# Performance work log

Measured on AMD Instinct MI355X. Metric: run time of the kernel, lower is better.

Reference implementation:

```python
import jax, jax.numpy as jnp
import numpy as np

N_USERS = 100000
N_ITEMS = 50000
N_ENTITIES = 180000
N_USER_NODES = 150000  # n_users + n_attributes
N_REL = 32
D = 64


def scatter_mean(src, index, num_segments):
    # torch_scatter scatter_mean: sum / count.clamp(min=1)
    s = jax.ops.segment_sum(src, index, num_segments=num_segments)
    cnt = jax.ops.segment_sum(jnp.ones((src.shape[0],), src.dtype), index, num_segments=num_segments)
    return s / jnp.clip(cnt, 1.0)[:, None]


def setup_inputs() -> dict:
    key = jax.random.key(0)
    ks = jax.random.split(key, 12)
    return {
        "entity_emb": jax.random.normal(ks[0], (N_ENTITIES, D), jnp.float32),
        "user_emb": jax.random.normal(ks[1], (N_USER_NODES, D), jnp.float32),
        "weight": jax.random.normal(ks[2], (N_REL, D), jnp.float32) * 0.1,
        "gate1_w": jax.random.normal(ks[3], (D, D), jnp.float32) * 0.1,
        "gate2_w": jax.random.normal(ks[4], (D, D), jnp.float32) * 0.1,
        "gate3_w": jax.random.normal(ks[5], (D, D), jnp.float32) * 0.1,
        "edge_index": jax.random.randint(ks[6], (2, 1500000), 0, N_ENTITIES, jnp.int32),
        "edge_type": jax.random.randint(ks[7], (1500000,), 0, N_REL, jnp.int32),
        "user_edge_index": jax.random.randint(ks[8], (2, 1000000), 0, N_USER_NODES, jnp.int32),
        "user_edge_type": jax.random.randint(ks[9], (1000000,), 0, N_REL, jnp.int32),
        "mat_row": jax.random.randint(ks[10], (1500000,), 0, N_USERS, jnp.int32),
        "mat_col": jax.random.randint(ks[11], (1500000,), 0, N_ITEMS, jnp.int32),
    }


def reference(entity_emb, user_emb, weight, gate1_w, gate2_w, gate3_w,
              edge_index, edge_type, user_edge_index, user_edge_type,
              mat_row, mat_col):
    # KG aggregate: gather tail + relation, multiply, scatter-mean to head
    head, tail = edge_index[0], edge_index[1]
    entity_agg = scatter_mean(entity_emb[tail] * weight[edge_type], head, N_ENTITIES)

    # UKG aggregate over the user+attribute graph
    uhead, utail = user_edge_index[0], user_edge_index[1]
    attribute_agg = scatter_mean(user_emb[utail] * weight[user_edge_type], uhead, N_USER_NODES)

    # user_gate: fuse KG item aggregation with user->item interaction aggregation
    item_kg_agg = entity_agg[:N_ITEMS]
    i_u_agg = scatter_mean(user_emb[mat_row] * weight[0], mat_col, N_ITEMS)
    gi = jax.nn.sigmoid(item_kg_agg @ gate1_w.T + i_u_agg @ gate2_w.T)
    item_emb_fusion = gi * item_kg_agg + (1.0 - gi) * i_u_agg

    # item_gate: fuse UKG user aggregation with item->user interaction aggregation
    user_ukg_agg = attribute_agg[:N_USERS]
    u_i_agg = scatter_mean(entity_emb[mat_col] * weight[0], mat_row, N_USERS)
    hi = jax.nn.sigmoid(u_i_agg @ gate2_w.T + user_ukg_agg @ gate3_w.T)
    user_emb_fusion = hi * user_ukg_agg + (1.0 - hi) * u_i_agg

    # forward output: fused item/user blocks concatenated with untouched tails
    entity_out = jnp.concatenate([item_emb_fusion, entity_agg[N_ITEMS:]], axis=0)
    user_out = jnp.concatenate([user_emb_fusion, attribute_agg[N_USERS:]], axis=0)
    return entity_out, user_out
```

## Files before the change

kernel.cpp:

```cpp
#include <hip/hip_runtime.h>

#define DD 64
#define NBKT 1024
#define CHUNK 8192
#define CAP_B 6656

struct SegCfg {
    int qbase[4];
    int rpb[4];
    float inv[4];
    int soff[4];
    int rows[4];
};

__global__ void __launch_bounds__(512, 2)
split_kernel(const int* __restrict__ dA, const int* __restrict__ sA, const int* __restrict__ tA,
             const int* __restrict__ dB, const int* __restrict__ sB, const int* __restrict__ tB,
             const int* __restrict__ dC, const int* __restrict__ sC,
             const int* __restrict__ dD, const int* __restrict__ sD,
             int nA, int nB, int nC, int nD,
             SegCfg cfg, int* __restrict__ gcur, unsigned long long* __restrict__ bkt) {
    __shared__ unsigned long long ord[CHUNK];
    __shared__ int cnt[NBKT];
    __shared__ int sc[NBKT];
    __shared__ int gb[NBKT];
    int t = threadIdx.x;
    int Etot = nA + nB + nC + nD;
    int base = blockIdx.x * CHUNK;
    if (base >= Etot) return;

    cnt[t] = 0; cnt[t + 512] = 0;
    __syncthreads();

    unsigned long long val[16];
    int qv[16], rv[16];
#pragma unroll
    for (int k = 0; k < 16; ++k) {
        int i = base + k * 512 + t;
        qv[k] = -1;
        if (i < Etot) {
            int j = i, d, seg, pv;
            if (j < nA)              { seg = 0; d = dA[j]; pv = sA[j] | (tA[j] << 20); }
            else if ((j -= nA) < nB) { seg = 1; d = dB[j]; pv = sB[j] | (tB[j] << 20); }
            else if ((j -= nB) < nC) { seg = 2; d = dC[j]; pv = sC[j]; }
            else { j -= nC;            seg = 3; d = dD[j]; pv = sD[j]; }
            int rpb = cfg.rpb[seg];
            int q = (int)((float)d * cfg.inv[seg]);
            if (d >= (q + 1) * rpb) ++q;
            else if (d < q * rpb) --q;
            int g = d + cfg.soff[seg];
            q += cfg.qbase[seg];
            val[k] = ((unsigned long long)q << 44) | ((unsigned long long)g << 25) | (unsigned)pv;
            qv[k] = q;
            rv[k] = atomicAdd(&cnt[q], 1);
        }
    }
    __syncthreads();

    int c0 = cnt[2 * t], c1 = cnt[2 * t + 1];
    {
        int s2 = c0 + c1;
        gb[t] = s2;
        __syncthreads();
        for (int off = 1; off < 512; off <<= 1) {
            int x = (t >= off) ? gb[t - off] : 0;
            __syncthreads();
            gb[t] += x;
            __syncthreads();
        }
        int run = gb[t] - s2;
        sc[2 * t] = run;
        sc[2 * t + 1] = run + c0;
    }
    __syncthreads();
    gb[2 * t]     = c0 ? atomicAdd(&gcur[2 * t], c0) : 0;
    gb[2 * t + 1] = c1 ? atomicAdd(&gcur[2 * t + 1], c1) : 0;
    __syncthreads();

#pragma unroll
    for (int k = 0; k < 16; ++k)
        if (qv[k] >= 0) ord[sc[qv[k]] + rv[k]] = val[k];
    __syncthreads();

    int tot = sc[NBKT - 1] + cnt[NBKT - 1];
    for (int i = t; i < tot; i += 512) {
        unsigned long long v = ord[i];
        int q = (int)(v >> 44);
        int idx = gb[q] + (i - sc[q]);
        if (idx < CAP_B)
            bkt[(size_t)q * CAP_B + idx] = v & 0xFFFFFFFFFFFULL;
    }
}

__global__ void __launch_bounds__(512, 2)
sort_gather(const unsigned long long* __restrict__ bkt, const int* __restrict__ gcur,
            SegCfg cfg,
            const float* __restrict__ entity_emb, const float* __restrict__ user_emb,
            const float* __restrict__ weight,
            float* __restrict__ out, float* __restrict__ usr_out,
            float* __restrict__ iu, float* __restrict__ ui) {
    __shared__ int cnt[1024];
    __shared__ int part[512];
    __shared__ int stage[CAP_B];
    int b = blockIdx.x, t = threadIdx.x;

    int seg = 0;
    if (b >= cfg.qbase[3]) seg = 3;
    else if (b >= cfg.qbase[2]) seg = 2;
    else if (b >= cfg.qbase[1]) seg = 1;
    int lb = b - cfg.qbase[seg];
    int row0 = cfg.soff[seg] + lb * cfg.rpb[seg];
    int nr = cfg.rows[seg] - lb * cfg.rpb[seg];
    if (nr > cfg.rpb[seg]) nr = cfg.rpb[seg];
    int n = gcur[b];
    if (n > CAP_B) n = CAP_B;
    const unsigned long long* src = bkt + (size_t)b * CAP_B;

    const float* emb = (seg == 0 || seg == 3) ? entity_emb : user_emb;
    float* dbase;
    if (seg == 0)      dbase = out     + (size_t)row0 * DD;
    else if (seg == 1) dbase = usr_out + (size_t)(row0 - cfg.soff[1]) * DD;
    else if (seg == 2) dbase = iu      + (size_t)(row0 - cfg.soff[2]) * DD;
    else               dbase = ui      + (size_t)(row0 - cfg.soff[3]) * DD;

    cnt[t] = 0; cnt[t + 512] = 0;
    __syncthreads();
    for (int i = t; i < n; i += 512) {
        int g = (int)(src[i] >> 25);
        atomicAdd(&cnt[g - row0], 1);
    }
    __syncthreads();

    {
        int c0 = cnt[2 * t], c1 = cnt[2 * t + 1];
        int s2 = c0 + c1;
        part[t] = s2;
        __syncthreads();
        for (int off = 1; off < 512; off <<= 1) {
            int y = (t >= off) ? part[t - off] : 0;
            __syncthreads();
            part[t] += y;
            __syncthreads();
        }
        int run = part[t] - s2;
        cnt[2 * t] = run;
        cnt[2 * t + 1] = run + c0;
    }
    __syncthreads();

    for (int i = t; i < n; i += 512) {
        unsigned long long v = src[i];
        int lr = (int)(v >> 25) - row0;
        int pos = atomicAdd(&cnt[lr], 1);
        stage[pos] = (int)(v & 0x1FFFFFF);
    }
    __syncthreads();

    int wv = t >> 6, lane = t & 63;
    for (int r = wv; r < nr; r += 8) {
        int start = (r == 0) ? 0 : cnt[r - 1];
        int end = cnt[r];
        float acc = 0.f;
        for (int base = start; base < end; base += 64) {
            int m = end - base; if (m > 64) m = 64;
            int pv = (lane < m) ? stage[base + lane] : 0;
            int j = 0;
            for (; j + 4 <= m; j += 4) {
                int p0 = __builtin_amdgcn_readlane(pv, j);
                int p1 = __builtin_amdgcn_readlane(pv, j + 1);
                int p2 = __builtin_amdgcn_readlane(pv, j + 2);
                int p3 = __builtin_amdgcn_readlane(pv, j + 3);
                const float* r0 = emb + (((unsigned)p0 & 0xFFFFFu) << 6);
                const float* r1 = emb + (((unsigned)p1 & 0xFFFFFu) << 6);
                const float* r2 = emb + (((unsigned)p2 & 0xFFFFFu) << 6);
                const float* r3 = emb + (((unsigned)p3 & 0xFFFFFu) << 6);
                float e0 = r0[lane], w0 = weight[(((unsigned)p0 >> 20) << 6) + lane];
                float e1 = r1[lane], w1 = weight[(((unsigned)p1 >> 20) << 6) + lane];
                float e2 = r2[lane], w2 = weight[(((unsigned)p2 >> 20) << 6) + lane];
                float e3 = r3[lane], w3 = weight[(((unsigned)p3 >> 20) << 6) + lane];
                acc += e0 * w0; acc += e1 * w1; acc += e2 * w2; acc += e3 * w3;
            }
            for (; j < m; ++j) {
                int pj = __builtin_amdgcn_readlane(pv, j);
                const float* rj = emb + (((unsigned)pj & 0xFFFFFu) << 6);
                acc += rj[lane] * weight[(((unsigned)pj >> 20) << 6) + lane];
            }
        }
        int deg = end - start;
        dbase[(size_t)r * DD + lane] = acc / (float)(deg > 0 ? deg : 1);
    }
}

__global__ void __launch_bounds__(256)
gate_fuse_kernel(const float* __restrict__ a_, const float* __restrict__ b_,
                 const float* __restrict__ gA, const float* __restrict__ gB,
                 float* __restrict__ out, int n_rows) {
    int lane = threadIdx.x & 63;
    float wa[DD], wb[DD];
    {
        const float4* ga4 = (const float4*)(gA + (lane << 6));
        const float4* gb4 = (const float4*)(gB + (lane << 6));
#pragma unroll
        for (int k4 = 0; k4 < 16; ++k4) {
            float4 va = ga4[k4];
            float4 vb = gb4[k4];
            wa[4 * k4 + 0] = va.x; wa[4 * k4 + 1] = va.y;
            wa[4 * k4 + 2] = va.z; wa[4 * k4 + 3] = va.w;
            wb[4 * k4 + 0] = vb.x; wb[4 * k4 + 1] = vb.y;
            wb[4 * k4 + 2] = vb.z; wb[4 * k4 + 3] = vb.w;
        }
    }
    int wid = blockIdx.x * (blockDim.x >> 6) + (threadIdx.x >> 6);
    int nw = gridDim.x * (blockDim.x >> 6);
    for (int row = wid; row < n_rows; row += nw) {
        int row_s = __builtin_amdgcn_readfirstlane(row);
        const float* ar = a_ + ((size_t)row_s << 6);
        const float* br = b_ + ((size_t)row_s << 6);
        float z = 0.f;
#pragma unroll
        for (int k = 0; k < DD; ++k) z = fmaf(ar[k], wa[k], z);
#pragma unroll
        for (int k = 0; k < DD; ++k) z = fmaf(br[k], wb[k], z);
        float g = 1.f / (1.f + expf(-z));
        float av = ar[lane], bv = br[lane];
        out[((size_t)row_s << 6) + lane] = g * av + (1.f - g) * bv;
    }
}

extern "C" void kernel_launch(void* const* d_in, const int* in_sizes, int n_in,
                              void* d_out, int out_size, void* d_ws, size_t ws_size,
                              hipStream_t stream) {
    const float* entity_emb = (const float*)d_in[0];
    const float* user_emb   = (const float*)d_in[1];
    const float* weight     = (const float*)d_in[2];
    const float* g1         = (const float*)d_in[3];
    const float* g2         = (const float*)d_in[4];
    const float* g3         = (const float*)d_in[5];
    const int* edge_index  = (const int*)d_in[6];
    const int* edge_type   = (const int*)d_in[7];
    const int* uedge_index = (const int*)d_in[8];
    const int* uedge_type  = (const int*)d_in[9];
    const int* mat_row     = (const int*)d_in[10];
    const int* mat_col     = (const int*)d_in[11];

    const int n_entities   = in_sizes[0] / DD;
    const int n_user_nodes = in_sizes[1] / DD;
    const int nA           = in_sizes[7];
    const int nB           = in_sizes[9];
    const int nM           = in_sizes[10];
    const int n_items      = 50000;
    const int n_users      = 100000;

    const int offB = n_entities;
    const int offC = offB + n_user_nodes;
    const int offD = offC + n_items;
    const int Etot = nA + nB + nM + nM;

    float* out      = (float*)d_out;
    float* user_out = out + (size_t)n_entities * DD;

    unsigned long long* bkt = (unsigned long long*)d_ws;
    int* gcur = (int*)(bkt + (size_t)NBKT * CAP_B);
    float* iu = (float*)(gcur + NBKT);
    float* ui = iu + (size_t)n_items * DD;

    SegCfg cfg;
    {
        int nb[4];
        nb[0] = (int)((long long)nA * NBKT / Etot);
        nb[1] = (int)((long long)nB * NBKT / Etot);
        nb[2] = (int)((long long)nM * NBKT / Etot);
        nb[3] = NBKT - nb[0] - nb[1] - nb[2];
        int rows[4] = {n_entities, n_user_nodes, n_items, n_users};
        int soff[4] = {0, offB, offC, offD};
        int qb = 0;
        for (int s = 0; s < 4; ++s) {
            cfg.qbase[s] = qb;
            cfg.rpb[s]   = (rows[s] + nb[s] - 1) / nb[s];
            cfg.inv[s]   = 1.0f / (float)cfg.rpb[s];
            cfg.soff[s]  = soff[s];
            cfg.rows[s]  = rows[s];
            qb += nb[s];
        }
    }

    hipMemsetAsync(gcur, 0, NBKT * sizeof(int), stream);

    int nchunk = (Etot + CHUNK - 1) / CHUNK;
    split_kernel<<<nchunk, 512, 0, stream>>>(edge_index, edge_index + nA, edge_type,
                                             uedge_index, uedge_index + nB, uedge_type,
                                             mat_col, mat_row,
                                             mat_row, mat_col,
                                             nA, nB, nM, nM, cfg, gcur, bkt);
    sort_gather<<<NBKT, 512, 0, stream>>>(bkt, gcur, cfg,
                                          entity_emb, user_emb, weight,
                                          out, user_out, iu, ui);

    gate_fuse_kernel<<<1024, 256, 0, stream>>>(out, iu, g1, g2, out, n_items);
    gate_fuse_kernel<<<1024, 256, 0, stream>>>(user_out, ui, g3, g2, user_out, n_users);
}
```

Measured before the change: 564.5 us.

## Two-pass bucket split without LDS staging to raise split_kernel occupancy

Rewrites split_kernel as two passes over the edge chunk. The first pass only counts entries per bucket, then the block reserves global ranges with atomics, and the second pass re-reads the inputs and writes each entry straight to its bucket slot using a shared per-bucket cursor. This removes the 64KB shared ordering buffer, the block-wide prefix scan and the per-thread register arrays, so the launch bound can go from 2 to 8 blocks per CU. The cost is reading the index arrays twice and losing the coalesced, bucket-ordered global writes.

```diff
diff --git a/kernel.cpp b/kernel.cpp
--- a/kernel.cpp
+++ b/kernel.cpp
@@ -13,16 +13,15 @@
     int rows[4];
 };
 
-__global__ void __launch_bounds__(512, 2)
+__global__ void __launch_bounds__(512, 8)
 split_kernel(const int* __restrict__ dA, const int* __restrict__ sA, const int* __restrict__ tA,
              const int* __restrict__ dB, const int* __restrict__ sB, const int* __restrict__ tB,
              const int* __restrict__ dC, const int* __restrict__ sC,
              const int* __restrict__ dD, const int* __restrict__ sD,
              int nA, int nB, int nC, int nD,
              SegCfg cfg, int* __restrict__ gcur, unsigned long long* __restrict__ bkt) {
-    __shared__ unsigned long long ord[CHUNK];
     __shared__ int cnt[NBKT];
-    __shared__ int sc[NBKT];
+    __shared__ int cur[NBKT];
     __shared__ int gb[NBKT];
     int t = threadIdx.x;
     int Etot = nA + nB + nC + nD;
@@ -30,65 +29,50 @@
     if (base >= Etot) return;
 
     cnt[t] = 0; cnt[t + 512] = 0;
-    __syncthreads();
-
-    unsigned long long val[16];
-    int qv[16], rv[16];
-#pragma unroll
+    cur[t] = 0; cur[t + 512] = 0;
+    __syncthreads();
+
     for (int k = 0; k < 16; ++k) {
         int i = base + k * 512 + t;
-        qv[k] = -1;
-        if (i < Etot) {
-            int j = i, d, seg, pv;
-            if (j < nA)              { seg = 0; d = dA[j]; pv = sA[j] | (tA[j] << 20); }
-            else if ((j -= nA) < nB) { seg = 1; d = dB[j]; pv = sB[j] | (tB[j] << 20); }
-            else if ((j -= nB) < nC) { seg = 2; d = dC[j]; pv = sC[j]; }
-            else { j -= nC;            seg = 3; d = dD[j]; pv = sD[j]; }
-            int rpb = cfg.rpb[seg];
-            int q = (int)((float)d * cfg.inv[seg]);
-            if (d >= (q + 1) * rpb) ++q;
-            else if (d < q * rpb) --q;
-            int g = d + cfg.soff[seg];
-            q += cfg.qbase[seg];
-            val[k] = ((unsigned long long)q << 44) | ((unsigned long long)g << 25) | (unsigned)pv;
-            qv[k] = q;
-            rv[k] = atomicAdd(&cnt[q], 1);
-        }
-    }
-    __syncthreads();
-
-    int c0 = cnt[2 * t], c1 = cnt[2 * t + 1];
-    {
-        int s2 = c0 + c1;
-        gb[t] = s2;
-        __syncthreads();
-        for (int off = 1; off < 512; off <<= 1) {
-            int x = (t >= off) ? gb[t - off] : 0;
-            __syncthreads();
-            gb[t] += x;
-            __syncthreads();
-        }
-        int run = gb[t] - s2;
-        sc[2 * t] = run;
-        sc[2 * t + 1] = run + c0;
-    }
-    __syncthreads();
-    gb[2 * t]     = c0 ? atomicAdd(&gcur[2 * t], c0) : 0;
-    gb[2 * t + 1] = c1 ? atomicAdd(&gcur[2 * t + 1], c1) : 0;
-    __syncthreads();
-
-#pragma unroll
-    for (int k = 0; k < 16; ++k)
-        if (qv[k] >= 0) ord[sc[qv[k]] + rv[k]] = val[k];
-    __syncthreads();
-
-    int tot = sc[NBKT - 1] + cnt[NBKT - 1];
-    for (int i = t; i < tot; i += 512) {
-        unsigned long long v = ord[i];
-        int q = (int)(v >> 44);
-        int idx = gb[q] + (i - sc[q]);
+        if (i >= Etot) break;
+        int j = i, d, seg;
+        if (j < nA)              { seg = 0; d = dA[j]; }
+        else if ((j -= nA) < nB) { seg = 1; d = dB[j]; }
+        else if ((j -= nB) < nC) { seg = 2; d = dC[j]; }
+        else { j -= nC;            seg = 3; d = dD[j]; }
+        int rpb = cfg.rpb[seg];
+        int q = (int)((float)d * cfg.inv[seg]);
+        if (d >= (q + 1) * rpb) ++q;
+        else if (d < q * rpb) --q;
+        atomicAdd(&cnt[q + cfg.qbase[seg]], 1);
+    }
+    __syncthreads();
+
+    {
+        int c0 = cnt[2 * t], c1 = cnt[2 * t + 1];
+        gb[2 * t]     = c0 ? atomicAdd(&gcur[2 * t], c0) : 0;
+        gb[2 * t + 1] = c1 ? atomicAdd(&gcur[2 * t + 1], c1) : 0;
+    }
+    __syncthreads();
+
+    for (int k = 0; k < 16; ++k) {
+        int i = base + k * 512 + t;
+        if (i >= Etot) break;
+        int j = i, d, seg, pv;
+        if (j < nA)              { seg = 0; d = dA[j]; pv = sA[j] | (tA[j] << 20); }
+        else if ((j -= nA) < nB) { seg = 1; d = dB[j]; pv = sB[j] | (tB[j] << 20); }
+        else if ((j -= nB) < nC) { seg = 2; d = dC[j]; pv = sC[j]; }
+        else { j -= nC;            seg = 3; d = dD[j]; pv = sD[j]; }
+        int rpb = cfg.rpb[seg];
+        int q = (int)((float)d * cfg.inv[seg]);
+        if (d >= (q + 1) * rpb) ++q;
+        else if (d < q * rpb) --q;
+        int g = d + cfg.soff[seg];
+        q += cfg.qbase[seg];
+        int pos = atomicAdd(&cur[q], 1);
+        int idx = gb[q] + pos;
         if (idx < CAP_B)
-            bkt[(size_t)q * CAP_B + idx] = v & 0xFFFFFFFFFFFULL;
+            bkt[(size_t)q * CAP_B + idx] = ((unsigned long long)g << 25) | (unsigned)pv;
     }
 }
 
```

Measured after the change: 618.7 us. 9.6% more time.
